# Kernel tuning notes

Hardware: AMD Instinct MI355X
Metric: run time of the kernel (lower is better)

Reference implementation:

```python
import jax, jax.numpy as jnp
import numpy as np

NUM_NODE = 64   # number of FPS nodes
NSAMPLE = 64    # ball-query / knn group size
RADIUS = 0.3    # first ball-query radius
K_INTERP = 3    # knn for upsample interpolation
BN_EPS = 1e-5


def sqdist(a, b):
    # a [B,S,3], b [B,N,3] -> squared distances [B,S,N]
    return (jnp.sum(a * a, -1)[:, :, None] + jnp.sum(b * b, -1)[:, None, :]
            - 2.0 * jnp.einsum('bsc,bnc->bsn', a, b))


def index_points(points, idx):
    # points [B,C,N] or [B,C,N,1]; idx [B,...] -> gathered [B,C,...]
    if points.ndim == 4:
        points = points[..., 0]
    return jax.vmap(lambda p, i: p[:, i])(points, idx)


def farthest_point_sample(xyz, npoint):
    # xyz [B,3,N] -> idx [B,npoint]; deterministic start at index 0
    B, C, N = xyz.shape

    def body(carry, _):
        dist, far = carry
        centroid = jnp.take_along_axis(xyz, far[:, None, None], axis=2)  # [B,3,1]
        d = jnp.sum((xyz - centroid) ** 2, axis=1)                       # [B,N]
        dist = jnp.minimum(dist, d)
        nxt = jnp.argmax(dist, axis=-1)
        return (dist, nxt), far

    init = (jnp.full((B, N), 1e10, xyz.dtype), jnp.zeros((B,), jnp.int32))
    _, idxs = jax.lax.scan(body, init, None, length=npoint)
    return idxs.T  # [B,npoint]


def query_ball_point(radius, nsample, xyz, new_xyz):
    # xyz [B,3,N], new_xyz [B,3,S] -> group idx [B,S,nsample]
    N = xyz.shape[2]
    sqr = sqdist(jnp.transpose(new_xyz, (0, 2, 1)), jnp.transpose(xyz, (0, 2, 1)))  # [B,S,N]
    if radius is not None:
        idx = jnp.broadcast_to(jnp.arange(N, dtype=jnp.int32), sqr.shape)
        idx = jnp.where(sqr > radius * radius, N, idx)
        idx = jnp.sort(idx, axis=-1)[:, :, :nsample]
        first = idx[:, :, :1]
        idx = jnp.where(idx == N, first, idx)  # pad misses with first hit
    else:
        idx = jnp.argsort(sqr, axis=-1)[:, :, :nsample].astype(jnp.int32)  # knn
    return idx


def _forward(input_fea, input_loc, pred_w, res_w, res_b, bn_gamma, bn_beta):
    # input_fea [B,C,N,1], input_loc [B,3,N]
    fidx = farthest_point_sample(input_loc, NUM_NODE)        # [B,S]
    fpoint_loc = index_points(input_loc, fidx)               # [B,3,S]
    fpoint_fea = index_points(input_fea, fidx)               # [B,C,S]

    gidx = query_ball_point(RADIUS, NSAMPLE, input_loc, fpoint_loc)  # [B,S,K]
    group_fea = index_points(input_fea, gidx) - fpoint_fea[..., None]  # [B,C,S,K]

    # pred_offset: 1x1 conv (no bias) + tanh
    seman = jnp.tanh(jnp.einsum('oc,bcsk->bosk', pred_w, group_fea))  # [B,3,S,K]

    group_loc = index_points(input_loc, gidx) - fpoint_loc[..., None]  # [B,3,S,K]
    node_offset = jnp.mean(seman * group_loc, axis=-1)       # [B,3,S]
    node_loc = fpoint_loc + node_offset                      # [B,3,S]

    gidx2 = query_ball_point(None, NSAMPLE, input_loc, node_loc)  # knn, [B,S,K]

    # residual branch: 1x1 conv + BatchNorm (training-mode batch stats) + ReLU
    res = jnp.einsum('oc,bcnk->bonk', res_w, input_fea) + res_b[None, :, None, None]
    mean = jnp.mean(res, axis=(0, 2, 3), keepdims=True)
    var = jnp.var(res, axis=(0, 2, 3), keepdims=True)
    res = (res - mean) * jax.lax.rsqrt(var + BN_EPS)
    res = jax.nn.relu(res * bn_gamma[None, :, None, None] + bn_beta[None, :, None, None])

    group_res = index_points(res, gidx2)                     # [B,F,S,K]
    node_fea = jnp.max(group_res, axis=-1, keepdims=True)    # [B,F,S,1]

    # upsample_inter: inverse-distance weighted 3-NN interpolation back to N points
    d = sqdist(jnp.transpose(input_loc, (0, 2, 1)), jnp.transpose(node_loc, (0, 2, 1)))  # [B,N,S]
    neg_d, kidx = jax.lax.top_k(-d, K_INTERP)                # k smallest dists
    dists = jnp.maximum(-neg_d, 1e-10)                       # [B,N,k]
    w = 1.0 / dists
    w = w / jnp.sum(w, axis=-1, keepdims=True)               # [B,N,k]
    interp = jnp.sum(index_points(node_fea, kidx) * w[:, None], axis=-1)  # [B,F,N]

    output_fea = jnp.concatenate([input_fea[..., 0], interp], axis=1)[..., None]  # [B,C+F,N,1]
    return output_fea, node_fea, node_offset


def setup_inputs() -> dict:
    key = jax.random.key(0)
    k1, k2, k3, k4, k5 = jax.random.split(key, 5)
    B, C, N = 32, 64, 8192
    FC = 64
    input_fea = jax.random.normal(k1, (B, C, N, 1), dtype=jnp.float32)
    input_loc = jax.random.uniform(k2, (B, 3, N), dtype=jnp.float32)
    pred_w = jax.random.normal(k3, (3, C), dtype=jnp.float32) * (1.0 / np.sqrt(C))
    res_w = jax.random.normal(k4, (FC, C), dtype=jnp.float32) * (1.0 / np.sqrt(C))
    res_b = jnp.zeros((FC,), dtype=jnp.float32)
    bn_gamma = jnp.ones((FC,), dtype=jnp.float32)
    bn_beta = jnp.zeros((FC,), dtype=jnp.float32)
    return {"input_fea": input_fea, "input_loc": input_loc, "pred_w": pred_w,
            "res_w": res_w, "res_b": res_b, "bn_gamma": bn_gamma, "bn_beta": bn_beta}


def reference(input_fea, input_loc, pred_w, res_w, res_b, bn_gamma, bn_beta):
    return _forward(input_fea, input_loc, pred_w, res_w, res_b, bn_gamma, bn_beta)
```

## Files before the change

kernel.cpp:

```cpp
#include <hip/hip_runtime.h>
#include <math.h>

#define BB 32
#define NN 8192
#define CC 64
#define SS 64
#define KK 64

#define WS_FIDX   0
#define WS_FLOC   2048
#define WS_FFEA   8192
#define WS_GIDX   139264
#define WS_NLOC   270336
#define WS_GIDX2  276480
#define WS_PART   407552
#define WS_TOT    2537472
#define WS_SCALE  2541632
#define WS_SHIFT  2541696


__device__ __forceinline__ void fps_body(int b, const float* __restrict__ loc,
                                         int* __restrict__ fidx,
                                         float (*wrv)[4], int (*wri)[4]) {
#pragma clang fp contract(off)
  int t = threadIdx.x;
  const float* lb = loc + (size_t)b * 3 * NN;
  float px[32], py[32], pz[32], dist[32];
#pragma unroll
  for (int k = 0; k < 32; k++) {
    int p = t + 256 * k;
    px[k] = lb[p];
    py[k] = lb[NN + p];
    pz[k] = lb[2 * NN + p];
    dist[k] = 1e10f;
  }
  int lane = t & 63, w = t >> 6;
  int far = 0;
  for (int it = 0; it < 64; it++) {
    if (t == 0) fidx[b * 64 + it] = far;
    int fs = __builtin_amdgcn_readfirstlane(far);
    float cx = lb[fs], cy = lb[NN + fs], cz = lb[2 * NN + fs];
    float bv = -1.0f; int bi = 0;
#pragma unroll
    for (int k = 0; k < 32; k++) {
      float dx = px[k] - cx, dy = py[k] - cy, dz = pz[k] - cz;
      float d = (dx * dx + dy * dy) + dz * dz;
      float dm = dist[k];
      dm = d < dm ? d : dm;
      dist[k] = dm;
      if (dm > bv) { bv = dm; bi = t + 256 * k; }
    }
    float v = bv; int vi = bi;
#pragma unroll
    for (int off = 1; off < 64; off <<= 1) {
      float v2 = __shfl_xor(v, off, 64);
      int   i2 = __shfl_xor(vi, off, 64);
      if (v2 > v || (v2 == v && i2 < vi)) { v = v2; vi = i2; }
    }
    int par = it & 1;
    if (lane == 0) { wrv[par][w] = v; wri[par][w] = vi; }
    __syncthreads();
    float gv = wrv[par][0]; int gi = wri[par][0];
#pragma unroll
    for (int w2 = 1; w2 < 4; w2++) {
      float v2 = wrv[par][w2]; int i2 = wri[par][w2];
      if (v2 > gv || (v2 == gv && i2 < gi)) { gv = v2; gi = i2; }
    }
    far = gi;
  }
}

__device__ __forceinline__ void transpose_body(int tb, const float* __restrict__ fea,
                                               float* __restrict__ feaT, float* tile) {
  int b = tb >> 7;
  int n0 = (tb & 127) * 64;
  int t = threadIdx.x;
  const float* fb = fea + (size_t)b * (CC * NN);
#pragma unroll
  for (int m = 0; m < 16; m++) {
    int idx = m * 256 + t;
    int c = idx >> 6, nl = idx & 63;
    tile[c * 65 + nl] = fb[(size_t)c * NN + n0 + nl];
  }
  __syncthreads();
  float* ob = feaT + ((size_t)b * NN + n0) * 64;
#pragma unroll
  for (int m = 0; m < 16; m++) {
    int idx = m * 256 + t;
    int nl = idx >> 6, c = idx & 63;
    ob[idx] = tile[c * 65 + nl];
  }
}

__device__ __forceinline__ void cov_body(int cb, const float* __restrict__ fea,
                                         float* __restrict__ part,
                                         float* Sf, float* red) {
  int t = threadIdx.x, w = t >> 6, lane = t & 63;
  int i = lane >> 3, j = lane & 7;
  float acc[8][8];
  float rs[8];
#pragma unroll
  for (int r = 0; r < 8; r++) {
    rs[r] = 0.f;
#pragma unroll
    for (int r2 = 0; r2 < 8; r2++) acc[r][r2] = 0.f;
  }
  for (int q = 0; q < 4; q++) {
    int chunk = cb * 4 + q;
    int p0 = chunk * 128;
    int b = p0 >> 13, n0 = p0 & 8191;
    __syncthreads();
    const float* fb = fea + (size_t)b * (CC * NN) + n0;
    for (int m = 0; m < 32; m++) {
      int idx = m * 256 + t;
      int c = idx >> 7, pt = idx & 127;
      Sf[c * 133 + pt] = fb[(size_t)c * NN + pt];
    }
    __syncthreads();
    for (int pt = w * 32; pt < w * 32 + 32; pt++) {
      float a[8], bv[8];
#pragma unroll
      for (int r = 0; r < 8; r++) {
        a[r] = Sf[(8 * i + r) * 133 + pt];
        bv[r] = Sf[(8 * j + r) * 133 + pt];
      }
#pragma unroll
      for (int r = 0; r < 8; r++) {
        rs[r] += a[r];
#pragma unroll
        for (int r2 = 0; r2 < 8; r2++) acc[r][r2] = fmaf(a[r], bv[r2], acc[r][r2]);
      }
    }
  }
  for (int ww = 0; ww < 4; ww++) {
    if (w == ww) {
#pragma unroll
      for (int r = 0; r < 8; r++) {
#pragma unroll
        for (int r2 = 0; r2 < 8; r2++) {
          int idx = (8 * i + r) * 64 + 8 * j + r2;
          if (ww == 0) red[idx] = acc[r][r2]; else red[idx] += acc[r][r2];
        }
        if (j == 0) {
          int ridx = 4096 + 8 * i + r;
          if (ww == 0) red[ridx] = rs[r]; else red[ridx] += rs[r];
        }
      }
    }
    __syncthreads();
  }
  float* pb = part + (size_t)cb * 4160;
  for (int idx = t; idx < 4160; idx += 256) pb[idx] = red[idx];
}

__global__ __launch_bounds__(256, 2) void phase1_kernel(const float* __restrict__ fea,
                                                        const float* __restrict__ loc,
                                                        float* __restrict__ feaT,
                                                        int* __restrict__ fidx,
                                                        float* __restrict__ part) {
  __shared__ __align__(16) char smem[50688];
  __shared__ float wrv[2][4];
  __shared__ int wri[2][4];
  int blk = blockIdx.x;
  if (blk < 32) {
    fps_body(blk, loc, fidx, wrv, wri);
  } else if (blk < 4128) {
    transpose_body(blk - 32, fea, feaT, (float*)smem);
  } else {
    cov_body(blk - 4128, fea, part, (float*)smem, (float*)(smem + 34048));
  }
}

__global__ __launch_bounds__(256) void phase2_kernel(const float* __restrict__ part,
                                                     float* __restrict__ tot,
                                                     const float* __restrict__ loc,
                                                     const float* __restrict__ fea,
                                                     const int* __restrict__ fidx,
                                                     float* __restrict__ floc,
                                                     float* __restrict__ ffea) {
  int blk = blockIdx.x, t = threadIdx.x;
  if (blk < 17) {
    int e = blk * 256 + t;
    if (e >= 4160) return;
    float s = 0.f;
    for (int b2 = 0; b2 < 512; b2++) s += part[(size_t)b2 * 4160 + e];
    tot[e] = s;
  } else {
    int bs = (blk - 17) * 4 + (t >> 6);
    int c = t & 63;
    int b = bs >> 6;
    int g = fidx[bs];
    ffea[bs * 64 + c] = fea[(size_t)b * (CC * NN) + (size_t)c * NN + g];
    if (c < 3) floc[bs * 3 + c] = loc[(size_t)b * (3 * NN) + (size_t)c * NN + g];
  }
}

__global__ __launch_bounds__(256) void phase3_kernel(const float* __restrict__ loc,
                                                     const float* __restrict__ floc,
                                                     int* __restrict__ gidx,
                                                     const float* __restrict__ tot,
                                                     const float* __restrict__ rw,
                                                     const float* __restrict__ rb,
                                                     const float* __restrict__ gam,
                                                     const float* __restrict__ bet,
                                                     float* __restrict__ bnsc,
                                                     float* __restrict__ bnsh) {
#pragma clang fp contract(off)
  int blk = blockIdx.x;
  if (blk < 512) {
    int w = threadIdx.x >> 6, lane = threadIdx.x & 63;
    int bs = blk * 4 + w, b = bs >> 6;
    const float* lb = loc + (size_t)b * 3 * NN;
    float ax = floc[bs * 3], ay = floc[bs * 3 + 1], az = floc[bs * 3 + 2];
    float A = (ax * ax + ay * ay) + az * az;
    int count = 0, firsth = -1;
    for (int ch = 0; ch < 128 && count < 64; ch++) {
      int p = ch * 64 + lane;
      float bx = lb[p], by = lb[NN + p], bz = lb[2 * NN + p];
      float Bn = (bx * bx + by * by) + bz * bz;
      float dot = fmaf(az, bz, fmaf(ay, by, ax * bx));
      float sqr = (A + Bn) - 2.0f * dot;
      bool hit = !(sqr > 0.09f);
      unsigned long long m = __ballot(hit);
      if (m) {
        if (firsth < 0) firsth = ch * 64 + (int)__ffsll(m) - 1;
        int pos = count + (int)__popcll(m & ((1ull << lane) - 1ull));
        if (hit && pos < 64) gidx[bs * 64 + pos] = p;
        count += (int)__popcll(m);
      }
    }
    if (count < 64 && lane >= count) gidx[bs * 64 + lane] = firsth;
  } else {
    int o = threadIdx.x;
    if (o >= 64) return;
    const float invM = 1.0f / 262144.0f;
    float mu = 0.f;
    for (int c = 0; c < 64; c++) mu += rw[o * 64 + c] * (tot[4096 + c] * invM);
    float exx = 0.f;
    for (int c = 0; c < 64; c++) {
      const float* row = tot + c * 64;
      float p = 0.f;
      for (int c2 = 0; c2 < 64; c2++) p += rw[o * 64 + c2] * row[c2];
      exx += rw[o * 64 + c] * p;
    }
    exx *= invM;
    float var = exx - mu * mu;
    float mean = mu + rb[o];
    float sc = gam[o] / sqrtf(var + 1e-5f);
    bnsc[o] = sc;
    bnsh[o] = bet[o] - mean * sc;
  }
}

__global__ __launch_bounds__(64) void seman_kernel(const float* __restrict__ feaT,
                                                   const float* __restrict__ loc,
                                                   const float* __restrict__ pw,
                                                   const int* __restrict__ gidx,
                                                   const float* __restrict__ ffea,
                                                   const float* __restrict__ floc,
                                                   float* __restrict__ out_noff,
                                                   float* __restrict__ nloc) {
  int bs = blockIdx.x, b = bs >> 6, s = bs & 63, k = threadIdx.x;
  __shared__ float sf[64];
  __shared__ float spw[192];
  __shared__ float sl[3];
  sf[k] = ffea[bs * 64 + k];
  spw[k] = pw[k]; spw[64 + k] = pw[64 + k]; spw[128 + k] = pw[128 + k];
  if (k < 3) sl[k] = floc[bs * 3 + k];
  __syncthreads();
  int g = gidx[bs * 64 + k];
  const float* fT = feaT + ((size_t)b * NN + g) * 64;
  float a0 = 0.f, a1 = 0.f, a2 = 0.f;
#pragma unroll
  for (int c4 = 0; c4 < 16; c4++) {
    float4 f = *(const float4*)(fT + 4 * c4);
    int c = 4 * c4;
    float g0 = f.x - sf[c + 0];
    a0 = fmaf(spw[c + 0], g0, a0); a1 = fmaf(spw[64 + c + 0], g0, a1); a2 = fmaf(spw[128 + c + 0], g0, a2);
    float g1 = f.y - sf[c + 1];
    a0 = fmaf(spw[c + 1], g1, a0); a1 = fmaf(spw[64 + c + 1], g1, a1); a2 = fmaf(spw[128 + c + 1], g1, a2);
    float g2 = f.z - sf[c + 2];
    a0 = fmaf(spw[c + 2], g2, a0); a1 = fmaf(spw[64 + c + 2], g2, a1); a2 = fmaf(spw[128 + c + 2], g2, a2);
    float g3 = f.w - sf[c + 3];
    a0 = fmaf(spw[c + 3], g3, a0); a1 = fmaf(spw[64 + c + 3], g3, a1); a2 = fmaf(spw[128 + c + 3], g3, a2);
  }
  const float* lb = loc + (size_t)b * 3 * NN;
  float c0 = tanhf(a0) * (lb[g] - sl[0]);
  float c1 = tanhf(a1) * (lb[NN + g] - sl[1]);
  float c2 = tanhf(a2) * (lb[2 * NN + g] - sl[2]);
#pragma unroll
  for (int off = 32; off; off >>= 1) {
    c0 += __shfl_xor(c0, off, 64);
    c1 += __shfl_xor(c1, off, 64);
    c2 += __shfl_xor(c2, off, 64);
  }
  if (k == 0) {
    float m0 = c0 * (1.0f / 64), m1 = c1 * (1.0f / 64), m2 = c2 * (1.0f / 64);
    out_noff[b * 192 + s] = m0;
    out_noff[b * 192 + 64 + s] = m1;
    out_noff[b * 192 + 128 + s] = m2;
    nloc[bs * 3 + 0] = sl[0] + m0;
    nloc[bs * 3 + 1] = sl[1] + m1;
    nloc[bs * 3 + 2] = sl[2] + m2;
  }
}

__global__ __launch_bounds__(256) void knn_kernel(const float* __restrict__ loc,
                                                  const float* __restrict__ nloc,
                                                  int* __restrict__ gidx2) {
#pragma clang fp contract(off)
  int bs = blockIdx.x, b = bs >> 6, t = threadIdx.x;
  const float* lb = loc + (size_t)b * 3 * NN;
  float ax = nloc[bs * 3], ay = nloc[bs * 3 + 1], az = nloc[bs * 3 + 2];
  float A = (ax * ax + ay * ay) + az * az;
  __shared__ unsigned keys[NN];
  __shared__ unsigned hist[4096];
  __shared__ unsigned part[256];
  __shared__ int sP, sC0, nOut, nCand;
  for (int m = 0; m < 16; m++) hist[m * 256 + t] = 0u;
  if (t == 0) { nOut = 0; nCand = 0; }
  __syncthreads();
  unsigned mykey[32];
#pragma unroll
  for (int k = 0; k < 32; k++) {
    int p = t + 256 * k;
    float bx = lb[p], by = lb[NN + p], bz = lb[2 * NN + p];
    float Bn = (bx * bx + by * by) + bz * bz;
    float dot = fmaf(az, bz, fmaf(ay, by, ax * bx));
    float d = (A + Bn) - 2.0f * dot;
    unsigned kb = __float_as_uint(d);
    kb = (kb & 0x80000000u) ? ~kb : (kb | 0x80000000u);
    mykey[k] = kb;
    keys[p] = kb;
    atomicAdd(&hist[kb >> 20], 1u);
  }
  __syncthreads();
  unsigned ps = 0;
#pragma unroll
  for (int m = 0; m < 16; m++) ps += hist[t * 16 + m];
  part[t] = ps;
  __syncthreads();
  if (t == 0) {
    int cum = 0, seg = 0;
    for (int t2 = 0; t2 < 256; t2++) {
      if (cum + (int)part[t2] >= 64) { seg = t2; break; }
      cum += (int)part[t2];
    }
    int P = seg * 16;
    for (;; P++) {
      if (cum + (int)hist[P] >= 64) break;
      cum += (int)hist[P];
    }
    sP = P; sC0 = cum;
  }
  __syncthreads();
  int P = sP, C0 = sC0;
  unsigned short* cand = (unsigned short*)hist;
  __syncthreads();
#pragma unroll
  for (int k = 0; k < 32; k++) {
    int bin = (int)(mykey[k] >> 20);
    if (bin < P) {
      int pos = atomicAdd(&nOut, 1);
      gidx2[bs * 64 + pos] = t + 256 * k;
    } else if (bin == P) {
      int c = atomicAdd(&nCand, 1);
      cand[c] = (unsigned short)(t + 256 * k);
    }
  }
  __syncthreads();
  if (t < 64) {
    int lane = t;
    int R = 64 - C0, nC = nCand;
    for (int r = 0; r < R; r++) {
      unsigned bk = 0xFFFFFFFFu; int bp = 0x7FFFFFFF, bj = -1;
      for (int j = lane; j < nC; j += 64) {
        int p = cand[j];
        if (p != 0xFFFF) {
          unsigned k2 = keys[p];
          if (k2 < bk || (k2 == bk && p < bp)) { bk = k2; bp = p; bj = j; }
        }
      }
#pragma unroll
      for (int off = 1; off < 64; off <<= 1) {
        unsigned k2 = __shfl_xor(bk, off, 64);
        int p2 = __shfl_xor(bp, off, 64);
        int j2 = __shfl_xor(bj, off, 64);
        if (k2 < bk || (k2 == bk && p2 < bp)) { bk = k2; bp = p2; bj = j2; }
      }
      if (lane == 0) {
        gidx2[bs * 64 + C0 + r] = bp;
        cand[bj] = 0xFFFF;
      }
      __threadfence_block();
    }
  }
}

__global__ __launch_bounds__(256) void nodefea_kernel(const float* __restrict__ feaT,
                                                      const float* __restrict__ rw,
                                                      const int* __restrict__ gidx2,
                                                      const float* __restrict__ bnsc,
                                                      const float* __restrict__ bnsh,
                                                      float* __restrict__ out_nf) {
  __shared__ __align__(16) float Lf[4096];
  __shared__ float Lw[4096];
  __shared__ int Lg[64];
  __shared__ float red[256];
  int bs = blockIdx.x, b = bs >> 6, s = bs & 63, t = threadIdx.x;
  if (t < 64) Lg[t] = gidx2[bs * 64 + t];
  __syncthreads();
#pragma unroll
  for (int m = 0; m < 4; m++) {
    int idx4 = m * 256 + t;
    int k = idx4 >> 4, c4 = idx4 & 15;
    float4 f = *(const float4*)(feaT + ((size_t)b * NN + Lg[k]) * 64 + 4 * c4);
    *(float4*)&Lf[idx4 * 4] = f;
  }
  for (int m = 0; m < 16; m++) {
    int idx = m * 256 + t;
    Lw[idx] = rw[(idx & 63) * 64 + (idx >> 6)];
  }
  __syncthreads();
  int o = t & 63, wq = t >> 6;
  float wreg[64];
#pragma unroll
  for (int c = 0; c < 64; c++) wreg[c] = Lw[c * 64 + o];
  float sc = bnsc[o], sh = bnsh[o];
  float mx = -1e30f;
  for (int k = wq * 16; k < wq * 16 + 16; k++) {
    float raw = 0.f;
#pragma unroll
    for (int c4 = 0; c4 < 16; c4++) {
      float4 lf = *(const float4*)&Lf[k * 64 + c4 * 4];
      raw = fmaf(wreg[4 * c4 + 0], lf.x, raw);
      raw = fmaf(wreg[4 * c4 + 1], lf.y, raw);
      raw = fmaf(wreg[4 * c4 + 2], lf.z, raw);
      raw = fmaf(wreg[4 * c4 + 3], lf.w, raw);
    }
    float v = raw * sc + sh;
    v = v > 0.f ? v : 0.f;
    mx = v > mx ? v : mx;
  }
  red[wq * 64 + o] = mx;
  __syncthreads();
  if (t < 64) {
    float m0 = red[t], m1 = red[64 + t], m2 = red[128 + t], m3 = red[192 + t];
    float ma = m0 > m1 ? m0 : m1;
    float mb = m2 > m3 ? m2 : m3;
    float m = ma > mb ? ma : mb;
    out_nf[b * 4096 + t * 64 + s] = m;
  }
}

__global__ __launch_bounds__(256) void interp_kernel(const float* __restrict__ fea,
                                                     const float* __restrict__ loc,
                                                     const float* __restrict__ nloc,
                                                     const float* __restrict__ nf,
                                                     float* __restrict__ out) {
#pragma clang fp contract(off)
  int b = blockIdx.y;
  int t = threadIdx.x;
  int n = blockIdx.x * 256 + t;
  __shared__ float snl[192];
  __shared__ float sB[64];
  if (t < 192) snl[t] = nloc[b * 192 + t];
  __syncthreads();
  if (t < 64) {
    float x = snl[t * 3], y = snl[t * 3 + 1], z = snl[t * 3 + 2];
    sB[t] = (x * x + y * y) + z * z;
  }
  __syncthreads();
  const float* lb = loc + (size_t)b * 3 * NN;
  float px = lb[n], py = lb[NN + n], pz = lb[2 * NN + n];
  float A = (px * px + py * py) + pz * pz;
  float d0 = 1e30f, d1 = 1e30f, d2 = 1e30f;
  int i0 = 0, i1 = 0, i2 = 0;
  for (int s = 0; s < 64; s++) {
    float dot = fmaf(pz, snl[s * 3 + 2], fmaf(py, snl[s * 3 + 1], px * snl[s * 3]));
    float d = (A + sB[s]) - 2.0f * dot;
    if (d < d0) { d2 = d1; i2 = i1; d1 = d0; i1 = i0; d0 = d; i0 = s; }
    else if (d < d1) { d2 = d1; i2 = i1; d1 = d; i1 = s; }
    else if (d < d2) { d2 = d; i2 = s; }
  }
  d0 = d0 > 1e-10f ? d0 : 1e-10f;
  d1 = d1 > 1e-10f ? d1 : 1e-10f;
  d2 = d2 > 1e-10f ? d2 : 1e-10f;
  float r0 = 1.0f / d0, r1 = 1.0f / d1, r2 = 1.0f / d2;
  float rsum = (r0 + r1) + r2;
  float w0 = r0 / rsum, w1 = r1 / rsum, w2 = r2 / rsum;
  const float* nfb = nf + b * 4096;
  const float* fb = fea + (size_t)b * (CC * NN);
  float* ob = out + (size_t)b * (128 * NN);
  for (int o = 0; o < 64; o++) {
    ob[(size_t)o * NN + n] = fb[(size_t)o * NN + n];
    float ip = (nfb[o * 64 + i0] * w0 + nfb[o * 64 + i1] * w1) + nfb[o * 64 + i2] * w2;
    ob[(size_t)(64 + o) * NN + n] = ip;
  }
}

extern "C" void kernel_launch(void* const* d_in, const int* in_sizes, int n_in,
                              void* d_out, int out_size, void* d_ws, size_t ws_size,
                              hipStream_t stream) {
  (void)in_sizes; (void)n_in; (void)out_size; (void)ws_size;
  const float* fea = (const float*)d_in[0];
  const float* loc = (const float*)d_in[1];
  const float* pw  = (const float*)d_in[2];
  const float* rw  = (const float*)d_in[3];
  const float* rb  = (const float*)d_in[4];
  const float* gam = (const float*)d_in[5];
  const float* bet = (const float*)d_in[6];
  float* out = (float*)d_out;
  float* ws = (float*)d_ws;

  int*   fidx  = (int*)(ws + WS_FIDX);
  float* floc  = ws + WS_FLOC;
  float* ffea  = ws + WS_FFEA;
  int*   gidx  = (int*)(ws + WS_GIDX);
  float* nlocp = ws + WS_NLOC;
  int*   gidx2 = (int*)(ws + WS_GIDX2);
  float* part  = ws + WS_PART;
  float* tot   = ws + WS_TOT;
  float* bnsc  = ws + WS_SCALE;
  float* bnsh  = ws + WS_SHIFT;

  float* feaT     = out;
  float* out_nf   = out + 33554432;
  float* out_noff = out + 33685504;

  phase1_kernel<<<dim3(4640), dim3(256), 0, stream>>>(fea, loc, feaT, fidx, part);
  phase2_kernel<<<dim3(529), dim3(256), 0, stream>>>(part, tot, loc, fea, fidx, floc, ffea);
  phase3_kernel<<<dim3(513), dim3(256), 0, stream>>>(loc, floc, gidx, tot, rw, rb, gam, bet, bnsc, bnsh);
  seman_kernel<<<dim3(2048), dim3(64), 0, stream>>>(feaT, loc, pw, gidx, ffea, floc, out_noff, nlocp);
  knn_kernel<<<dim3(2048), dim3(256), 0, stream>>>(loc, nlocp, gidx2);
  nodefea_kernel<<<dim3(2048), dim3(256), 0, stream>>>(feaT, rw, gidx2, bnsc, bnsh, out_nf);
  interp_kernel<<<dim3(32, 32), dim3(256), 0, stream>>>(fea, loc, nlocp, out_nf, out);
}
```

Baseline: 564.1 us.

## Fuse ball query, semantic offset and knn into one kernel; widen FPS blocks

New measurement: 604.9 us. +7.2%, slower.

```diff
diff --git a/kernel.cpp b/kernel.cpp
--- a/kernel.cpp
+++ b/kernel.cpp
@@ -8,9 +8,6 @@
 #define KK 64
 
 #define WS_FIDX   0
-#define WS_FLOC   2048
-#define WS_FFEA   8192
-#define WS_GIDX   139264
 #define WS_NLOC   270336
 #define WS_GIDX2  276480
 #define WS_PART   407552
@@ -21,14 +18,17 @@
 
 __device__ __forceinline__ void fps_body(int b, const float* __restrict__ loc,
                                          int* __restrict__ fidx,
-                                         float (*wrv)[4], int (*wri)[4]) {
+                                         float (*wrv)[8], int (*wri)[8],
+                                         float (*wrx)[8], float (*wry)[8],
+                                         float (*wrz)[8]) {
 #pragma clang fp contract(off)
+  __builtin_amdgcn_s_setprio(1);
   int t = threadIdx.x;
   const float* lb = loc + (size_t)b * 3 * NN;
-  float px[32], py[32], pz[32], dist[32];
-#pragma unroll
-  for (int k = 0; k < 32; k++) {
-    int p = t + 256 * k;
+  float px[16], py[16], pz[16], dist[16];
+#pragma unroll
+  for (int k = 0; k < 16; k++) {
+    int p = t + 512 * k;
     px[k] = lb[p];
     py[k] = lb[NN + p];
     pz[k] = lb[2 * NN + p];
@@ -36,37 +36,49 @@
   }
   int lane = t & 63, w = t >> 6;
   int far = 0;
+  float cx = lb[0], cy = lb[NN], cz = lb[2 * NN];
   for (int it = 0; it < 64; it++) {
     if (t == 0) fidx[b * 64 + it] = far;
-    int fs = __builtin_amdgcn_readfirstlane(far);
-    float cx = lb[fs], cy = lb[NN + fs], cz = lb[2 * NN + fs];
     float bv = -1.0f; int bi = 0;
-#pragma unroll
-    for (int k = 0; k < 32; k++) {
+    float bx = 0.f, by = 0.f, bz = 0.f;
+#pragma unroll
+    for (int k = 0; k < 16; k++) {
       float dx = px[k] - cx, dy = py[k] - cy, dz = pz[k] - cz;
       float d = (dx * dx + dy * dy) + dz * dz;
       float dm = dist[k];
       dm = d < dm ? d : dm;
       dist[k] = dm;
-      if (dm > bv) { bv = dm; bi = t + 256 * k; }
+      if (dm > bv) { bv = dm; bi = t + 512 * k; bx = px[k]; by = py[k]; bz = pz[k]; }
     }
     float v = bv; int vi = bi;
+    float vx = bx, vy = by, vz = bz;
 #pragma unroll
     for (int off = 1; off < 64; off <<= 1) {
       float v2 = __shfl_xor(v, off, 64);
       int   i2 = __shfl_xor(vi, off, 64);
-      if (v2 > v || (v2 == v && i2 < vi)) { v = v2; vi = i2; }
+      float x2 = __shfl_xor(vx, off, 64);
+      float y2 = __shfl_xor(vy, off, 64);
+      float z2 = __shfl_xor(vz, off, 64);
+      if (v2 > v || (v2 == v && i2 < vi)) { v = v2; vi = i2; vx = x2; vy = y2; vz = z2; }
     }
     int par = it & 1;
-    if (lane == 0) { wrv[par][w] = v; wri[par][w] = vi; }
+    if (lane == 0) {
+      wrv[par][w] = v; wri[par][w] = vi;
+      wrx[par][w] = vx; wry[par][w] = vy; wrz[par][w] = vz;
+    }
     __syncthreads();
     float gv = wrv[par][0]; int gi = wri[par][0];
-#pragma unroll
-    for (int w2 = 1; w2 < 4; w2++) {
+    float gx = wrx[par][0], gy = wry[par][0], gz = wrz[par][0];
+#pragma unroll
+    for (int w2 = 1; w2 < 8; w2++) {
       float v2 = wrv[par][w2]; int i2 = wri[par][w2];
-      if (v2 > gv || (v2 == gv && i2 < gi)) { gv = v2; gi = i2; }
+      if (v2 > gv || (v2 == gv && i2 < gi)) {
+        gv = v2; gi = i2;
+        gx = wrx[par][w2]; gy = wry[par][w2]; gz = wrz[par][w2];
+      }
     }
     far = gi;
+    cx = gx; cy = gy; cz = gz;
   }
 }
 
@@ -77,16 +89,16 @@
   int t = threadIdx.x;
   const float* fb = fea + (size_t)b * (CC * NN);
 #pragma unroll
-  for (int m = 0; m < 16; m++) {
-    int idx = m * 256 + t;
+  for (int m = 0; m < 8; m++) {
+    int idx = m * 512 + t;
     int c = idx >> 6, nl = idx & 63;
     tile[c * 65 + nl] = fb[(size_t)c * NN + n0 + nl];
   }
   __syncthreads();
   float* ob = feaT + ((size_t)b * NN + n0) * 64;
 #pragma unroll
-  for (int m = 0; m < 16; m++) {
-    int idx = m * 256 + t;
+  for (int m = 0; m < 8; m++) {
+    int idx = m * 512 + t;
     int nl = idx >> 6, c = idx & 63;
     ob[idx] = tile[c * 65 + nl];
   }
@@ -111,24 +123,26 @@
     int b = p0 >> 13, n0 = p0 & 8191;
     __syncthreads();
     const float* fb = fea + (size_t)b * (CC * NN) + n0;
-    for (int m = 0; m < 32; m++) {
-      int idx = m * 256 + t;
+    for (int m = 0; m < 16; m++) {
+      int idx = m * 512 + t;
       int c = idx >> 7, pt = idx & 127;
       Sf[c * 133 + pt] = fb[(size_t)c * NN + pt];
     }
     __syncthreads();
-    for (int pt = w * 32; pt < w * 32 + 32; pt++) {
-      float a[8], bv[8];
-#pragma unroll
-      for (int r = 0; r < 8; r++) {
-        a[r] = Sf[(8 * i + r) * 133 + pt];
-        bv[r] = Sf[(8 * j + r) * 133 + pt];
-      }
-#pragma unroll
-      for (int r = 0; r < 8; r++) {
-        rs[r] += a[r];
-#pragma unroll
-        for (int r2 = 0; r2 < 8; r2++) acc[r][r2] = fmaf(a[r], bv[r2], acc[r][r2]);
+    if (w < 4) {
+      for (int pt = w * 32; pt < w * 32 + 32; pt++) {
+        float a[8], bv[8];
+#pragma unroll
+        for (int r = 0; r < 8; r++) {
+          a[r] = Sf[(8 * i + r) * 133 + pt];
+          bv[r] = Sf[(8 * j + r) * 133 + pt];
+        }
+#pragma unroll
+        for (int r = 0; r < 8; r++) {
+          rs[r] += a[r];
+#pragma unroll
+          for (int r2 = 0; r2 < 8; r2++) acc[r][r2] = fmaf(a[r], bv[r2], acc[r][r2]);
+        }
       }
     }
   }
@@ -150,20 +164,20 @@
     __syncthreads();
   }
   float* pb = part + (size_t)cb * 4160;
-  for (int idx = t; idx < 4160; idx += 256) pb[idx] = red[idx];
-}
-
-__global__ __launch_bounds__(256, 2) void phase1_kernel(const float* __restrict__ fea,
+  for (int idx = t; idx < 4160; idx += 512) pb[idx] = red[idx];
+}
+
+__global__ __launch_bounds__(512, 1) void phase1_kernel(const float* __restrict__ fea,
                                                         const float* __restrict__ loc,
                                                         float* __restrict__ feaT,
                                                         int* __restrict__ fidx,
                                                         float* __restrict__ part) {
   __shared__ __align__(16) char smem[50688];
-  __shared__ float wrv[2][4];
-  __shared__ int wri[2][4];
+  __shared__ float wrv[2][8], wrx[2][8], wry[2][8], wrz[2][8];
+  __shared__ int wri[2][8];
   int blk = blockIdx.x;
   if (blk < 32) {
-    fps_body(blk, loc, fidx, wrv, wri);
+    fps_body(blk, loc, fidx, wrv, wri, wrx, wry, wrz);
   } else if (blk < 4128) {
     transpose_body(blk - 32, fea, feaT, (float*)smem);
   } else {
@@ -171,47 +185,49 @@
   }
 }
 
-__global__ __launch_bounds__(256) void phase2_kernel(const float* __restrict__ part,
-                                                     float* __restrict__ tot,
-                                                     const float* __restrict__ loc,
-                                                     const float* __restrict__ fea,
-                                                     const int* __restrict__ fidx,
-                                                     float* __restrict__ floc,
-                                                     float* __restrict__ ffea) {
-  int blk = blockIdx.x, t = threadIdx.x;
-  if (blk < 17) {
-    int e = blk * 256 + t;
-    if (e >= 4160) return;
-    float s = 0.f;
-    for (int b2 = 0; b2 < 512; b2++) s += part[(size_t)b2 * 4160 + e];
-    tot[e] = s;
-  } else {
-    int bs = (blk - 17) * 4 + (t >> 6);
-    int c = t & 63;
-    int b = bs >> 6;
-    int g = fidx[bs];
-    ffea[bs * 64 + c] = fea[(size_t)b * (CC * NN) + (size_t)c * NN + g];
-    if (c < 3) floc[bs * 3 + c] = loc[(size_t)b * (3 * NN) + (size_t)c * NN + g];
-  }
-}
-
-__global__ __launch_bounds__(256) void phase3_kernel(const float* __restrict__ loc,
-                                                     const float* __restrict__ floc,
-                                                     int* __restrict__ gidx,
-                                                     const float* __restrict__ tot,
-                                                     const float* __restrict__ rw,
-                                                     const float* __restrict__ rb,
-                                                     const float* __restrict__ gam,
-                                                     const float* __restrict__ bet,
-                                                     float* __restrict__ bnsc,
-                                                     float* __restrict__ bnsh) {
+__global__ __launch_bounds__(256) void mega_kernel(const float* __restrict__ loc,
+                                                   const float* __restrict__ feaT,
+                                                   const float* __restrict__ pw,
+                                                   const int* __restrict__ fidx,
+                                                   const float* __restrict__ part,
+                                                   float* __restrict__ tot,
+                                                   int* __restrict__ gidx2,
+                                                   float* __restrict__ out_noff,
+                                                   float* __restrict__ nloc) {
 #pragma clang fp contract(off)
   int blk = blockIdx.x;
-  if (blk < 512) {
-    int w = threadIdx.x >> 6, lane = threadIdx.x & 63;
-    int bs = blk * 4 + w, b = bs >> 6;
-    const float* lb = loc + (size_t)b * 3 * NN;
-    float ax = floc[bs * 3], ay = floc[bs * 3 + 1], az = floc[bs * 3 + 2];
+  if (blk >= 2048) {
+    int e = (blk - 2048) * 256 + threadIdx.x;
+    if (e < 4160) {
+      float sum = 0.f;
+      for (int b2 = 0; b2 < 512; b2++) sum += part[(size_t)b2 * 4160 + e];
+      tot[e] = sum;
+    }
+    return;
+  }
+  int bs = blk, b = bs >> 6, s = bs & 63, t = threadIdx.x;
+  int lane = t & 63, w = t >> 6;
+  __shared__ unsigned keys[NN];
+  __shared__ unsigned hist[4096];
+  __shared__ unsigned partl[256];
+  __shared__ float sf[64];
+  __shared__ float spw[192];
+  __shared__ float sl[3];
+  __shared__ float sA[3];
+  __shared__ int gidxL[64];
+  __shared__ int sP, sC0, nOut, nCand;
+  const float* lb = loc + (size_t)b * 3 * NN;
+
+  if (t < 192) spw[t] = pw[t];
+  if (w == 0) {
+    int g = fidx[bs];
+    sf[lane] = feaT[((size_t)b * NN + g) * 64 + lane];
+    if (lane < 3) sl[lane] = lb[(size_t)lane * NN + g];
+  }
+  __syncthreads();
+
+  if (w == 0) {
+    float ax = sl[0], ay = sl[1], az = sl[2];
     float A = (ax * ax + ay * ay) + az * az;
     int count = 0, firsth = -1;
     for (int ch = 0; ch < 128 && count < 64; ch++) {
@@ -225,98 +241,56 @@
       if (m) {
         if (firsth < 0) firsth = ch * 64 + (int)__ffsll(m) - 1;
         int pos = count + (int)__popcll(m & ((1ull << lane) - 1ull));
-        if (hit && pos < 64) gidx[bs * 64 + pos] = p;
+        if (hit && pos < 64) gidxL[pos] = p;
         count += (int)__popcll(m);
       }
     }
-    if (count < 64 && lane >= count) gidx[bs * 64 + lane] = firsth;
-  } else {
-    int o = threadIdx.x;
-    if (o >= 64) return;
-    const float invM = 1.0f / 262144.0f;
-    float mu = 0.f;
-    for (int c = 0; c < 64; c++) mu += rw[o * 64 + c] * (tot[4096 + c] * invM);
-    float exx = 0.f;
-    for (int c = 0; c < 64; c++) {
-      const float* row = tot + c * 64;
-      float p = 0.f;
-      for (int c2 = 0; c2 < 64; c2++) p += rw[o * 64 + c2] * row[c2];
-      exx += rw[o * 64 + c] * p;
-    }
-    exx *= invM;
-    float var = exx - mu * mu;
-    float mean = mu + rb[o];
-    float sc = gam[o] / sqrtf(var + 1e-5f);
-    bnsc[o] = sc;
-    bnsh[o] = bet[o] - mean * sc;
-  }
-}
-
-__global__ __launch_bounds__(64) void seman_kernel(const float* __restrict__ feaT,
-                                                   const float* __restrict__ loc,
-                                                   const float* __restrict__ pw,
-                                                   const int* __restrict__ gidx,
-                                                   const float* __restrict__ ffea,
-                                                   const float* __restrict__ floc,
-                                                   float* __restrict__ out_noff,
-                                                   float* __restrict__ nloc) {
-  int bs = blockIdx.x, b = bs >> 6, s = bs & 63, k = threadIdx.x;
-  __shared__ float sf[64];
-  __shared__ float spw[192];
-  __shared__ float sl[3];
-  sf[k] = ffea[bs * 64 + k];
-  spw[k] = pw[k]; spw[64 + k] = pw[64 + k]; spw[128 + k] = pw[128 + k];
-  if (k < 3) sl[k] = floc[bs * 3 + k];
-  __syncthreads();
-  int g = gidx[bs * 64 + k];
-  const float* fT = feaT + ((size_t)b * NN + g) * 64;
-  float a0 = 0.f, a1 = 0.f, a2 = 0.f;
-#pragma unroll
-  for (int c4 = 0; c4 < 16; c4++) {
-    float4 f = *(const float4*)(fT + 4 * c4);
-    int c = 4 * c4;
-    float g0 = f.x - sf[c + 0];
-    a0 = fmaf(spw[c + 0], g0, a0); a1 = fmaf(spw[64 + c + 0], g0, a1); a2 = fmaf(spw[128 + c + 0], g0, a2);
-    float g1 = f.y - sf[c + 1];
-    a0 = fmaf(spw[c + 1], g1, a0); a1 = fmaf(spw[64 + c + 1], g1, a1); a2 = fmaf(spw[128 + c + 1], g1, a2);
-    float g2 = f.z - sf[c + 2];
-    a0 = fmaf(spw[c + 2], g2, a0); a1 = fmaf(spw[64 + c + 2], g2, a1); a2 = fmaf(spw[128 + c + 2], g2, a2);
-    float g3 = f.w - sf[c + 3];
-    a0 = fmaf(spw[c + 3], g3, a0); a1 = fmaf(spw[64 + c + 3], g3, a1); a2 = fmaf(spw[128 + c + 3], g3, a2);
-  }
-  const float* lb = loc + (size_t)b * 3 * NN;
-  float c0 = tanhf(a0) * (lb[g] - sl[0]);
-  float c1 = tanhf(a1) * (lb[NN + g] - sl[1]);
-  float c2 = tanhf(a2) * (lb[2 * NN + g] - sl[2]);
-#pragma unroll
-  for (int off = 32; off; off >>= 1) {
-    c0 += __shfl_xor(c0, off, 64);
-    c1 += __shfl_xor(c1, off, 64);
-    c2 += __shfl_xor(c2, off, 64);
-  }
-  if (k == 0) {
-    float m0 = c0 * (1.0f / 64), m1 = c1 * (1.0f / 64), m2 = c2 * (1.0f / 64);
-    out_noff[b * 192 + s] = m0;
-    out_noff[b * 192 + 64 + s] = m1;
-    out_noff[b * 192 + 128 + s] = m2;
-    nloc[bs * 3 + 0] = sl[0] + m0;
-    nloc[bs * 3 + 1] = sl[1] + m1;
-    nloc[bs * 3 + 2] = sl[2] + m2;
-  }
-}
-
-__global__ __launch_bounds__(256) void knn_kernel(const float* __restrict__ loc,
-                                                  const float* __restrict__ nloc,
-                                                  int* __restrict__ gidx2) {
-#pragma clang fp contract(off)
-  int bs = blockIdx.x, b = bs >> 6, t = threadIdx.x;
-  const float* lb = loc + (size_t)b * 3 * NN;
-  float ax = nloc[bs * 3], ay = nloc[bs * 3 + 1], az = nloc[bs * 3 + 2];
+    if (count < 64 && lane >= count) gidxL[lane] = firsth;
+  }
+  __syncthreads();
+
+  if (w == 0) {
+    int g = gidxL[lane];
+    const float* fT = feaT + ((size_t)b * NN + g) * 64;
+    float a0 = 0.f, a1 = 0.f, a2 = 0.f;
+#pragma unroll
+    for (int c4 = 0; c4 < 16; c4++) {
+      float4 f = *(const float4*)(fT + 4 * c4);
+      int c = 4 * c4;
+      float g0 = f.x - sf[c + 0];
+      a0 = fmaf(spw[c + 0], g0, a0); a1 = fmaf(spw[64 + c + 0], g0, a1); a2 = fmaf(spw[128 + c + 0], g0, a2);
+      float g1 = f.y - sf[c + 1];
+      a0 = fmaf(spw[c + 1], g1, a0); a1 = fmaf(spw[64 + c + 1], g1, a1); a2 = fmaf(spw[128 + c + 1], g1, a2);
+      float g2 = f.z - sf[c + 2];
+      a0 = fmaf(spw[c + 2], g2, a0); a1 = fmaf(spw[64 + c + 2], g2, a1); a2 = fmaf(spw[128 + c + 2], g2, a2);
+      float g3 = f.w - sf[c + 3];
+      a0 = fmaf(spw[c + 3], g3, a0); a1 = fmaf(spw[64 + c + 3], g3, a1); a2 = fmaf(spw[128 + c + 3], g3, a2);
+    }
+    float c0 = tanhf(a0) * (lb[g] - sl[0]);
+    float c1 = tanhf(a1) * (lb[NN + g] - sl[1]);
+    float c2 = tanhf(a2) * (lb[2 * NN + g] - sl[2]);
+#pragma unroll
+    for (int off = 32; off; off >>= 1) {
+      c0 += __shfl_xor(c0, off, 64);
+      c1 += __shfl_xor(c1, off, 64);
+      c2 += __shfl_xor(c2, off, 64);
+    }
+    if (lane == 0) {
+      float m0 = c0 * (1.0f / 64), m1 = c1 * (1.0f / 64), m2 = c2 * (1.0f / 64);
+      out_noff[b * 192 + s] = m0;
+      out_noff[b * 192 + 64 + s] = m1;
+      out_noff[b * 192 + 128 + s] = m2;
+      float nx = sl[0] + m0, ny = sl[1] + m1, nz = sl[2] + m2;
+      nloc[bs * 3 + 0] = nx;
+      nloc[bs * 3 + 1] = ny;
+      nloc[bs * 3 + 2] = nz;
+      sA[0] = nx; sA[1] = ny; sA[2] = nz;
+    }
+  }
+  __syncthreads();
+
+  float ax = sA[0], ay = sA[1], az = sA[2];
   float A = (ax * ax + ay * ay) + az * az;
-  __shared__ unsigned keys[NN];
-  __shared__ unsigned hist[4096];
-  __shared__ unsigned part[256];
-  __shared__ int sP, sC0, nOut, nCand;
   for (int m = 0; m < 16; m++) hist[m * 256 + t] = 0u;
   if (t == 0) { nOut = 0; nCand = 0; }
   __syncthreads();
@@ -338,13 +312,13 @@
   unsigned ps = 0;
 #pragma unroll
   for (int m = 0; m < 16; m++) ps += hist[t * 16 + m];
-  part[t] = ps;
+  partl[t] = ps;
   __syncthreads();
   if (t == 0) {
     int cum = 0, seg = 0;
     for (int t2 = 0; t2 < 256; t2++) {
-      if (cum + (int)part[t2] >= 64) { seg = t2; break; }
-      cum += (int)part[t2];
+      if (cum + (int)partl[t2] >= 64) { seg = t2; break; }
+      cum += (int)partl[t2];
     }
     int P = seg * 16;
     for (;; P++) {
@@ -370,7 +344,6 @@
   }
   __syncthreads();
   if (t < 64) {
-    int lane = t;
     int R = 64 - C0, nC = nCand;
     for (int r = 0; r < R; r++) {
       unsigned bk = 0xFFFFFFFFu; int bp = 0x7FFFFFFF, bj = -1;
@@ -395,6 +368,32 @@
       __threadfence_block();
     }
   }
+}
+
+__global__ __launch_bounds__(64) void bnstats_kernel(const float* __restrict__ tot,
+                                                     const float* __restrict__ rw,
+                                                     const float* __restrict__ rb,
+                                                     const float* __restrict__ gam,
+                                                     const float* __restrict__ bet,
+                                                     float* __restrict__ bnsc,
+                                                     float* __restrict__ bnsh) {
+  int o = threadIdx.x;
+  const float invM = 1.0f / 262144.0f;
+  float mu = 0.f;
+  for (int c = 0; c < 64; c++) mu += rw[o * 64 + c] * (tot[4096 + c] * invM);
+  float exx = 0.f;
+  for (int c = 0; c < 64; c++) {
+    const float* row = tot + c * 64;
+    float p = 0.f;
+    for (int c2 = 0; c2 < 64; c2++) p += rw[o * 64 + c2] * row[c2];
+    exx += rw[o * 64 + c] * p;
+  }
+  exx *= invM;
+  float var = exx - mu * mu;
+  float mean = mu + rb[o];
+  float sc = gam[o] / sqrtf(var + 1e-5f);
+  bnsc[o] = sc;
+  bnsh[o] = bet[o] - mean * sc;
 }
 
 __global__ __launch_bounds__(256) void nodefea_kernel(const float* __restrict__ feaT,
@@ -514,9 +513,6 @@
   float* ws = (float*)d_ws;
 
   int*   fidx  = (int*)(ws + WS_FIDX);
-  float* floc  = ws + WS_FLOC;
-  float* ffea  = ws + WS_FFEA;
-  int*   gidx  = (int*)(ws + WS_GIDX);
   float* nlocp = ws + WS_NLOC;
   int*   gidx2 = (int*)(ws + WS_GIDX2);
   float* part  = ws + WS_PART;
@@ -528,11 +524,10 @@
   float* out_nf   = out + 33554432;
   float* out_noff = out + 33685504;
 
-  phase1_kernel<<<dim3(4640), dim3(256), 0, stream>>>(fea, loc, feaT, fidx, part);
-  phase2_kernel<<<dim3(529), dim3(256), 0, stream>>>(part, tot, loc, fea, fidx, floc, ffea);
-  phase3_kernel<<<dim3(513), dim3(256), 0, stream>>>(loc, floc, gidx, tot, rw, rb, gam, bet, bnsc, bnsh);
-  seman_kernel<<<dim3(2048), dim3(64), 0, stream>>>(feaT, loc, pw, gidx, ffea, floc, out_noff, nlocp);
-  knn_kernel<<<dim3(2048), dim3(256), 0, stream>>>(loc, nlocp, gidx2);
+  phase1_kernel<<<dim3(4640), dim3(512), 0, stream>>>(fea, loc, feaT, fidx, part);
+  mega_kernel<<<dim3(2065), dim3(256), 0, stream>>>(loc, feaT, pw, fidx, part, tot,
+                                                    gidx2, out_noff, nlocp);
+  bnstats_kernel<<<dim3(1), dim3(64), 0, stream>>>(tot, rw, rb, gam, bet, bnsc, bnsh);
   nodefea_kernel<<<dim3(2048), dim3(256), 0, stream>>>(feaT, rw, gidx2, bnsc, bnsh, out_nf);
   interp_kernel<<<dim3(32, 32), dim3(256), 0, stream>>>(fea, loc, nlocp, out_nf, out);
 }
```
